# Performance work log

Measured on AMD Instinct MI355X. Metric: run time of the kernel, lower is better.

## Reference

```python
import jax, jax.numpy as jnp
import numpy as np

PHI = (1.0 + np.sqrt(5.0)) / 2.0
B, S, D, N, L, H, V = 2, 1024, 128, 256, 2, 2, 32000


def _euler_scan(w_emb, b_emb, positions):
    # w_emb, b_emb: (B,S,D); sequential complex-rotation recurrence over S
    Bq, Sq, Dq = w_emb.shape

    def step(carry, xs):
        h_real, h_imag = carry
        w_t, b_t, pos = xs  # (B,D), (B,D), ()
        wl = 1.0 + jnp.abs(w_t)
        t_phi = pos * PHI
        th_r = h_real / wl + b_t + t_phi
        th_i = h_imag / wl + b_t + t_phi
        sr, cr = jnp.sin(th_r), jnp.cos(th_r)
        si, ci = jnp.sin(th_i), jnp.cos(th_i)
        nr = cr * ci - sr * si
        ni = cr * si + sr * ci
        return (nr, ni), (nr, ni)

    init = (jnp.zeros((Bq, Dq), w_emb.dtype), jnp.zeros((Bq, Dq), w_emb.dtype))
    xs = (jnp.swapaxes(w_emb, 0, 1), jnp.swapaxes(b_emb, 0, 1), positions)
    _, (reals, imags) = jax.lax.scan(step, init, xs)
    return jnp.swapaxes(reals, 0, 1), jnp.swapaxes(imags, 0, 1)


def _echo_head(states_real, states_imag, positions, w_q, b_q, alpha_p):
    Bq, Sq, Dq = states_real.shape
    scale = jnp.sqrt(jnp.asarray(2.0 * Dq, states_real.dtype))
    wl_q = 1.0 + jnp.abs(w_q)
    t_phi = (positions * PHI)[None, :, None]
    th_r = states_real / wl_q + b_q + t_phi
    th_i = states_imag / wl_q + b_q + t_phi
    Q = jnp.concatenate([jnp.cos(th_r), jnp.cos(th_i)], axis=-1)  # (B,S,2D)
    K = jnp.concatenate([states_real, states_imag], axis=-1)      # (B,S,2D)
    scores = jnp.einsum('bqd,bkd->bqk', Q, K) / scale
    causal = jnp.triu(jnp.ones((Sq, Sq), bool), k=1)
    scores = jnp.where(causal[None], -jnp.inf, scores)
    scores = scores.at[:, 0, 0].set(0.0)
    attn = jax.nn.softmax(scores, axis=-1)
    retrieved = jnp.einsum('bqk,bkd->bqd', attn, K)  # (B,S,2D)
    alpha = jax.nn.sigmoid(alpha_p)

    def ema_step(ema, x_t):
        ema = alpha * x_t + (1.0 - alpha) * ema
        return ema, ema

    _, ema_states = jax.lax.scan(ema_step,
                                 jnp.zeros((Bq, 2 * Dq), retrieved.dtype),
                                 jnp.swapaxes(retrieved, 0, 1))
    ema_states = jnp.swapaxes(ema_states, 0, 1)  # (B,S,2D)
    return ema_states[..., :Dq] + ema_states[..., Dq:]


def _echo_module(states_real, states_imag, positions, w_q, b_q, alpha_p, w_out, b_out):
    # w_q,b_q: (H,D); alpha_p: (H,)
    heads = jax.vmap(_echo_head, in_axes=(None, None, None, 0, 0, 0))(
        states_real, states_imag, positions, w_q, b_q, alpha_p)
    combined = heads.sum(axis=0)  # interference sum over heads
    wl_out = 1.0 + jnp.abs(w_out)
    theta = combined / wl_out + b_out
    return jnp.cos(theta) + jnp.sin(theta)


def _resonant_ffn(x, W, Bp, attn_cos, attn_sin, proj_cos, proj_sin):
    # x: (B,S,D); W,Bp,attn_*: (N,D); proj_*: (D,N)
    theta = x[..., None, :] / (1.0 + jnp.abs(W)) + Bp  # (B,S,N,D)
    cos_sum = jnp.sum(jnp.cos(theta) * attn_cos, axis=-1)  # (B,S,N)
    sin_sum = jnp.sum(jnp.sin(theta) * attn_sin, axis=-1)
    out = cos_sum @ proj_cos.T + sin_sum @ proj_sin.T  # (B,S,D)
    return jax.nn.silu(out)


def setup_inputs() -> dict:
    key = jax.random.key(0)
    ks = jax.random.split(key, 16)
    f32 = jnp.float32
    return {
        'input_ids': jax.random.randint(ks[0], (B, S), 0, V),
        'embed': jax.random.normal(ks[1], (V, 2 * D), f32) * 0.02,
        'wq': jax.random.normal(ks[2], (L, H, D), f32) * 0.02,
        'bq': jnp.zeros((L, H, D), f32),
        'alpha': jnp.full((L, H), 0.1, f32),
        'wout': jax.random.normal(ks[3], (L, D), f32) * 0.02,
        'bout': jnp.zeros((L, D), f32),
        'ffn_W': jax.random.normal(ks[4], (L, N, D), f32) * 0.02,
        'ffn_B': jnp.zeros((L, N, D), f32),
        'attn_cos': jnp.ones((L, N, D), f32),
        'attn_sin': jnp.ones((L, N, D), f32),
        'proj_cos': jax.random.uniform(ks[5], (L, D, N), f32, -0.05, 0.05),
        'proj_sin': jax.random.uniform(ks[6], (L, D, N), f32, -0.05, 0.05),
        'echo_scales': jnp.full((L,), 0.5, f32),
        'res_scales': jnp.full((L,), 0.5, f32),
        'out_proj': jax.random.normal(ks[7], (V, D), f32) * 0.02,
    }


def reference(input_ids, embed, wq, bq, alpha, wout, bout, ffn_W, ffn_B,
              attn_cos, attn_sin, proj_cos, proj_sin, echo_scales, res_scales,
              out_proj):
    emb = embed[input_ids]  # (B,S,2D)
    Dq = emb.shape[-1] // 2
    w_emb, b_emb = emb[..., :Dq], emb[..., Dq:]
    positions = jnp.arange(emb.shape[1], dtype=emb.dtype)
    sr, si = _euler_scan(w_emb, b_emb, positions)
    x = sr + si
    for l in range(wq.shape[0]):
        echo = _echo_module(sr, si, positions, wq[l], bq[l], alpha[l], wout[l], bout[l])
        res = _resonant_ffn(x, ffn_W[l], ffn_B[l], attn_cos[l], attn_sin[l],
                            proj_cos[l], proj_sin[l])
        x = x + (echo_scales[l] * echo + res_scales[l] * res)
    return x @ out_proj.T  # (B,S,V)
```

## Files before the change

kernel.cpp:

```cpp
#include <hip/hip_runtime.h>
#include <math.h>

#define B_ 2
#define S_ 1024
#define D_ 128
#define N_ 256
#define L_ 2
#define H_ 2
#define V_ 32000

#define INV2PI 0.15915494309189535f
#define PHI_F 1.61803398874989484f

__device__ __forceinline__ float fract_(float x) { return x - floorf(x); }
__device__ __forceinline__ float fsin_(float th) { return __builtin_amdgcn_sinf(fract_(th * INV2PI)); }
__device__ __forceinline__ float fcos_(float th) { return __builtin_amdgcn_cosf(fract_(th * INV2PI)); }

typedef __bf16 bf16x8 __attribute__((ext_vector_type(8)));
typedef float f32x4 __attribute__((ext_vector_type(4)));

__global__ __launch_bounds__(256) void k_gp(const int* __restrict__ ids, const float* __restrict__ embed,
                                            float* __restrict__ eg,
                                            const float* __restrict__ W, const float* __restrict__ Bp,
                                            const float* __restrict__ ac, const float* __restrict__ as2,
                                            const float* __restrict__ pc, const float* __restrict__ ps,
                                            float* __restrict__ iwT, float* __restrict__ bpT,
                                            float* __restrict__ acT, float* __restrict__ asT,
                                            float* __restrict__ pcT, float* __restrict__ psT) {
    int blk = blockIdx.x;
    if (blk < 2048) {
        int i = blk * 256 + threadIdx.x;
        int c = i & 255, t = (i >> 8) & 1023, b = i >> 18;
        eg[i] = embed[(size_t)ids[b * S_ + t] * 256 + c];
    } else {
        int i = (blk - 2048) * 256 + threadIdx.x;
        int d = i & 127, n = (i >> 7) & 255, l = i >> 15;
        int ti = (l * 128 + d) * 256 + n;
        iwT[ti] = 1.f / (1.f + fabsf(W[i]));
        bpT[ti] = Bp[i];
        acT[ti] = ac[i];
        asT[ti] = as2[i];
        pcT[(l * 256 + n) * 128 + d] = pc[ti];
        psT[(l * 256 + n) * 128 + d] = ps[ti];
    }
}

__global__ __launch_bounds__(128) void k_euler(const float* __restrict__ eg,
                                               float* __restrict__ sr, float* __restrict__ si,
                                               float* __restrict__ x,
                                               __bf16* __restrict__ Kh, __bf16* __restrict__ Kl,
                                               __bf16* __restrict__ KTh, __bf16* __restrict__ KTl) {
    int b = blockIdx.x;
    int d = threadIdx.x;
    const float* p0 = eg + (size_t)b * S_ * 256 + d;
    float h = 0.f;
    double tp = 0.0;
    const double DTP = 2.0 * 1.6180339887498949;
    const double TWO_PI = 6.283185307179586476925286766559;
    float wA[8], bA[8], wB[8], bB[8];
#pragma unroll
    for (int k = 0; k < 8; ++k) { wA[k] = p0[k * 256]; bA[k] = p0[k * 256 + 128]; }
    for (int g = 0; g < 128; ++g) {
        if (g < 127) {
            const float* p = p0 + (size_t)(g + 1) * 8 * 256;
#pragma unroll
            for (int k = 0; k < 8; ++k) { wB[k] = p[k * 256]; bB[k] = p[k * 256 + 128]; }
        }
#pragma unroll
        for (int k = 0; k < 8; ++k) {
            int t = g * 8 + k;
            float inv = 1.f / (1.f + fabsf(wA[k]));
            float th = fmaf(h, inv, 2.f * bA[k] + (float)tp);
            float u = fract_(th * INV2PI);
            float sn = __builtin_amdgcn_sinf(u);
            float cs = __builtin_amdgcn_cosf(u);
            size_t idx = ((size_t)b * S_ + t) * D_ + d;
            sr[idx] = cs; si[idx] = sn; x[idx] = cs + sn;
            __bf16 ch = (__bf16)cs; __bf16 cl = (__bf16)(cs - (float)ch);
            __bf16 sh2 = (__bf16)sn; __bf16 sl = (__bf16)(sn - (float)sh2);
            size_t ki = ((size_t)b * S_ + t) * 256 + d;
            Kh[ki] = ch; Kl[ki] = cl;
            Kh[ki + 128] = sh2; Kl[ki + 128] = sl;
            size_t kt1 = ((size_t)b * 256 + d) * S_ + t;
            size_t kt2 = ((size_t)b * 256 + d + 128) * S_ + t;
            KTh[kt1] = ch; KTl[kt1] = cl;
            KTh[kt2] = sh2; KTl[kt2] = sl;
            h = cs + sn;
            tp += DTP; if (tp >= TWO_PI) tp -= TWO_PI;
        }
#pragma unroll
        for (int k = 0; k < 8; ++k) { wA[k] = wB[k]; bA[k] = bB[k]; }
    }
}

__global__ __launch_bounds__(256) void k_qq(const float* __restrict__ sr, const float* __restrict__ si,
                                            const float* __restrict__ wq, const float* __restrict__ bq,
                                            __bf16* __restrict__ Qh0, __bf16* __restrict__ Ql0,
                                            __bf16* __restrict__ Qh1, __bf16* __restrict__ Ql1) {
    int i = blockIdx.x * 256 + threadIdx.x;
    int l = i >> 20;
    int j = i & 0xFFFFF;
    int c = j & 255;
    int s = (j >> 8) & 1023;
    int bh = j >> 18;
    int h = bh & 1, b = bh >> 1;
    int d = c & 127;
    const float* st = (c < 128) ? sr : si;
    float v = st[((size_t)b * S_ + s) * D_ + d];
    float w = wq[(l * H_ + h) * D_ + d], bb = bq[(l * H_ + h) * D_ + d];
    float th = v / (1.f + fabsf(w)) + bb + (float)s * PHI_F;
    float qv = fcos_(th);
    __bf16 hq = (__bf16)qv;
    __bf16 lq = (__bf16)(qv - (float)hq);
    if (l == 0) { Qh0[j] = hq; Ql0[j] = lq; }
    else        { Qh1[j] = hq; Ql1[j] = lq; }
}

#define LSTR 40

__global__ __launch_bounds__(256) void k_scores_mfma(const __bf16* __restrict__ Qh, const __bf16* __restrict__ Ql,
                                                     const __bf16* __restrict__ Kh, const __bf16* __restrict__ Kl,
                                                     float* __restrict__ sc) {
    int kt = blockIdx.x, qt = blockIdx.y, bh = blockIdx.z;
    if (kt > qt) return;
    __shared__ __bf16 Ah[128 * LSTR], Al[128 * LSTR], Bh[128 * LSTR], Bl[128 * LSTR];
    int tid = threadIdx.x;
    int wid = tid >> 6, lane = tid & 63;
    int wy = wid >> 1, wx = wid & 1;
    int fl = lane & 15, qq = lane >> 4;
    int srow = tid >> 1, sseg = (tid & 1) * 16;
    const __bf16* qh = Qh + ((size_t)bh * S_ + qt * 128 + srow) * 256 + sseg;
    const __bf16* ql = Ql + ((size_t)bh * S_ + qt * 128 + srow) * 256 + sseg;
    const __bf16* kh = Kh + ((size_t)(bh >> 1) * S_ + kt * 128 + srow) * 256 + sseg;
    const __bf16* kl = Kl + ((size_t)(bh >> 1) * S_ + kt * 128 + srow) * 256 + sseg;
    int lbase = srow * LSTR + sseg;

    f32x4 acc[4][4];
#pragma unroll
    for (int i = 0; i < 4; ++i)
#pragma unroll
        for (int j = 0; j < 4; ++j) { acc[i][j][0] = 0.f; acc[i][j][1] = 0.f; acc[i][j][2] = 0.f; acc[i][j][3] = 0.f; }

    for (int kc = 0; kc < 256; kc += 32) {
        uint4 a0 = *(const uint4*)(qh + kc); uint4 a1 = *(const uint4*)(qh + kc + 8);
        uint4 l0 = *(const uint4*)(ql + kc); uint4 l1 = *(const uint4*)(ql + kc + 8);
        uint4 b0 = *(const uint4*)(kh + kc); uint4 b1 = *(const uint4*)(kh + kc + 8);
        uint4 c0 = *(const uint4*)(kl + kc); uint4 c1 = *(const uint4*)(kl + kc + 8);
        __syncthreads();
        *(uint4*)&Ah[lbase] = a0; *(uint4*)&Ah[lbase + 8] = a1;
        *(uint4*)&Al[lbase] = l0; *(uint4*)&Al[lbase + 8] = l1;
        *(uint4*)&Bh[lbase] = b0; *(uint4*)&Bh[lbase + 8] = b1;
        *(uint4*)&Bl[lbase] = c0; *(uint4*)&Bl[lbase + 8] = c1;
        __syncthreads();
        bf16x8 fah[4], fal[4], fbh[4], fbl[4];
#pragma unroll
        for (int tm = 0; tm < 4; ++tm) {
            int r = (wy * 64 + tm * 16 + fl) * LSTR + qq * 8;
            fah[tm] = *(const bf16x8*)&Ah[r];
            fal[tm] = *(const bf16x8*)&Al[r];
        }
#pragma unroll
        for (int tn = 0; tn < 4; ++tn) {
            int r = (wx * 64 + tn * 16 + fl) * LSTR + qq * 8;
            fbh[tn] = *(const bf16x8*)&Bh[r];
            fbl[tn] = *(const bf16x8*)&Bl[r];
        }
#pragma unroll
        for (int tm = 0; tm < 4; ++tm)
#pragma unroll
            for (int tn = 0; tn < 4; ++tn) {
                acc[tm][tn] = __builtin_amdgcn_mfma_f32_16x16x32_bf16(fah[tm], fbh[tn], acc[tm][tn], 0, 0, 0);
                acc[tm][tn] = __builtin_amdgcn_mfma_f32_16x16x32_bf16(fah[tm], fbl[tn], acc[tm][tn], 0, 0, 0);
                acc[tm][tn] = __builtin_amdgcn_mfma_f32_16x16x32_bf16(fal[tm], fbh[tn], acc[tm][tn], 0, 0, 0);
            }
    }
    const float s16 = 0.0625f;
    float* Cp = sc + (size_t)bh * S_ * S_;
    int grow0 = qt * 128 + wy * 64 + qq * 4;
    int gcol0 = kt * 128 + wx * 64 + fl;
#pragma unroll
    for (int tm = 0; tm < 4; ++tm)
#pragma unroll
        for (int tn = 0; tn < 4; ++tn) {
            size_t base = (size_t)(grow0 + tm * 16) * S_ + gcol0 + tn * 16;
#pragma unroll
            for (int r = 0; r < 4; ++r)
                Cp[base + (size_t)r * S_] = acc[tm][tn][r] * s16;
        }
}

__global__ __launch_bounds__(256) void k_pv_sm(const float* __restrict__ SCf,
                                               const __bf16* __restrict__ KTh, const __bf16* __restrict__ KTl,
                                               float* __restrict__ R) {
    __shared__ __bf16 Ah[128 * LSTR], Al[128 * LSTR], Bh[128 * LSTR], Bl[128 * LSTR];
    __shared__ float mrow[128], rrow[128];
    int nt = blockIdx.x, qt = blockIdx.y, bh = blockIdx.z;
    int tid = threadIdx.x;
    int wid = tid >> 6, lane = tid & 63;
    int wy = wid >> 1, wx = wid & 1;
    int fl = lane & 15, qq = lane >> 4;
    int srow = tid >> 1, half = tid & 1, sseg = half * 16;
    const float* Sp = SCf + (size_t)bh * S_ * S_;
    int kceil = qt * 128 + 128;
    {
        int r = srow;
        int q = qt * 128 + r;
        const float* rp = Sp + (size_t)q * S_;
        float m = -3e38f;
        for (int c = half * 4; c < kceil; c += 8) {
            float4 v = *(const float4*)&rp[c];
            if (c + 0 <= q) m = fmaxf(m, v.x);
            if (c + 1 <= q) m = fmaxf(m, v.y);
            if (c + 2 <= q) m = fmaxf(m, v.z);
            if (c + 3 <= q) m = fmaxf(m, v.w);
        }
        m = fmaxf(m, __shfl_xor(m, 1));
        float s = 0.f;
        for (int c = half * 4; c < kceil; c += 8) {
            float4 v = *(const float4*)&rp[c];
            if (c + 0 <= q) s += __expf(v.x - m);
            if (c + 1 <= q) s += __expf(v.y - m);
            if (c + 2 <= q) s += __expf(v.z - m);
            if (c + 3 <= q) s += __expf(v.w - m);
        }
        s += __shfl_xor(s, 1);
        mrow[r] = m;
        rrow[r] = 1.f / s;
    }
    __syncthreads();
    float mR = mrow[srow], rsR = rrow[srow];
    int qrow = qt * 128 + srow;
    const float* ap = Sp + (size_t)qrow * S_ + sseg;
    const __bf16* bh_p = KTh + ((size_t)(bh >> 1) * 256 + nt * 128 + srow) * S_ + sseg;
    const __bf16* bl_p = KTl + ((size_t)(bh >> 1) * 256 + nt * 128 + srow) * S_ + sseg;
    int lbase = srow * LSTR + sseg;

    f32x4 acc[4][4];
#pragma unroll
    for (int i = 0; i < 4; ++i)
#pragma unroll
        for (int j = 0; j < 4; ++j) { acc[i][j][0] = 0.f; acc[i][j][1] = 0.f; acc[i][j][2] = 0.f; acc[i][j][3] = 0.f; }

    for (int kc = 0; kc < kceil; kc += 32) {
        float4 f0 = *(const float4*)(ap + kc);
        float4 f1 = *(const float4*)(ap + kc + 4);
        float4 f2 = *(const float4*)(ap + kc + 8);
        float4 f3 = *(const float4*)(ap + kc + 12);
        uint4 b0 = *(const uint4*)(bh_p + kc); uint4 b1 = *(const uint4*)(bh_p + kc + 8);
        uint4 c0 = *(const uint4*)(bl_p + kc); uint4 c1 = *(const uint4*)(bl_p + kc + 8);
        float vv[16] = {f0.x, f0.y, f0.z, f0.w, f1.x, f1.y, f1.z, f1.w,
                        f2.x, f2.y, f2.z, f2.w, f3.x, f3.y, f3.z, f3.w};
        bf16x8 h0, h1, l0, l1;
#pragma unroll
        for (int e = 0; e < 16; ++e) {
            int col = kc + sseg + e;
            float p = (col <= qrow) ? __expf(vv[e] - mR) * rsR : 0.f;
            __bf16 hi = (__bf16)p;
            __bf16 lo = (__bf16)(p - (float)hi);
            if (e < 8) { h0[e] = hi; l0[e] = lo; }
            else       { h1[e - 8] = hi; l1[e - 8] = lo; }
        }
        __syncthreads();
        *(bf16x8*)&Ah[lbase] = h0; *(bf16x8*)&Ah[lbase + 8] = h1;
        *(bf16x8*)&Al[lbase] = l0; *(bf16x8*)&Al[lbase + 8] = l1;
        *(uint4*)&Bh[lbase] = b0; *(uint4*)&Bh[lbase + 8] = b1;
        *(uint4*)&Bl[lbase] = c0; *(uint4*)&Bl[lbase + 8] = c1;
        __syncthreads();
        bf16x8 fah[4], fal[4], fbh[4], fbl[4];
#pragma unroll
        for (int tm = 0; tm < 4; ++tm) {
            int r = (wy * 64 + tm * 16 + fl) * LSTR + qq * 8;
            fah[tm] = *(const bf16x8*)&Ah[r];
            fal[tm] = *(const bf16x8*)&Al[r];
        }
#pragma unroll
        for (int tn = 0; tn < 4; ++tn) {
            int r = (wx * 64 + tn * 16 + fl) * LSTR + qq * 8;
            fbh[tn] = *(const bf16x8*)&Bh[r];
            fbl[tn] = *(const bf16x8*)&Bl[r];
        }
#pragma unroll
        for (int tm = 0; tm < 4; ++tm)
#pragma unroll
            for (int tn = 0; tn < 4; ++tn) {
                acc[tm][tn] = __builtin_amdgcn_mfma_f32_16x16x32_bf16(fah[tm], fbh[tn], acc[tm][tn], 0, 0, 0);
                acc[tm][tn] = __builtin_amdgcn_mfma_f32_16x16x32_bf16(fah[tm], fbl[tn], acc[tm][tn], 0, 0, 0);
                acc[tm][tn] = __builtin_amdgcn_mfma_f32_16x16x32_bf16(fal[tm], fbh[tn], acc[tm][tn], 0, 0, 0);
            }
    }
    float* Rp = R + (size_t)bh * S_ * 256;
    int grow0 = qt * 128 + wy * 64 + qq * 4;
    int gcol0 = nt * 128 + wx * 64 + fl;
#pragma unroll
    for (int tm = 0; tm < 4; ++tm)
#pragma unroll
        for (int tn = 0; tn < 4; ++tn) {
            size_t base = (size_t)(grow0 + tm * 16) * 256 + gcol0 + tn * 16;
#pragma unroll
            for (int r = 0; r < 4; ++r)
                Rp[base + (size_t)r * 256] = acc[tm][tn][r];
        }
}

#define TROWS 4
__global__ __launch_bounds__(256) void k_tail(const float* __restrict__ R,
                                              const float* __restrict__ apar,
                                              float* __restrict__ x,
                                              const float* __restrict__ iwT, const float* __restrict__ bpT,
                                              const float* __restrict__ acT, const float* __restrict__ asT,
                                              const float* __restrict__ pcT, const float* __restrict__ psT,
                                              const float* __restrict__ wout, const float* __restrict__ bout,
                                              const float* __restrict__ esp, const float* __restrict__ rsp,
                                              __bf16* __restrict__ Xh, __bf16* __restrict__ Xl, int last) {
    int blk = blockIdx.x;
    int row0 = blk * TROWS;
    int b = row0 >> 10, t0 = row0 & 1023;
    int tid = threadIdx.x;
    __shared__ float wsh[2][64];
    __shared__ float emah[TROWS][256];
    __shared__ float xs[TROWS][128];
    __shared__ float csh[TROWS][256], ssh[TROWS][256];
    if (tid < 128) {
        int h = tid >> 6, j = tid & 63;
        float a = 1.f / (1.f + __expf(-apar[h]));
        wsh[h][j] = a * exp2f((float)j * log2f(1.f - a));
    }
    {
        int i0 = tid;
        xs[i0 >> 7][i0 & 127] = x[(size_t)row0 * D_ + i0];
        int i1 = tid + 256;
        xs[i1 >> 7][i1 & 127] = x[(size_t)row0 * D_ + i1];
    }
    __syncthreads();
    {
        int dim = tid;
        if (t0 >= 63) {
#pragma unroll
            for (int r = 0; r < TROWS; ++r) {
                int t = t0 + r;
                float acc = 0.f;
#pragma unroll
                for (int h = 0; h < 2; ++h) {
                    const float* base = R + ((size_t)(b * 2 + h) * S_ + t) * 256 + dim;
                    float s = 0.f;
#pragma unroll
                    for (int j = 0; j < 64; ++j) s = fmaf(wsh[h][j], base[-j * 256], s);
                    acc += s;
                }
                emah[r][dim] = acc;
            }
        } else {
            for (int r = 0; r < TROWS; ++r) {
                int t = t0 + r;
                int jm = t < 63 ? t : 63;
                float acc = 0.f;
                for (int h = 0; h < 2; ++h) {
                    const float* base = R + ((size_t)(b * 2 + h) * S_ + t) * 256 + dim;
                    float s = 0.f;
                    for (int j = 0; j <= jm; ++j) s = fmaf(wsh[h][j], base[-j * 256], s);
                    acc += s;
                }
                emah[r][dim] = acc;
            }
        }
    }
    __syncthreads();
    {
        int n = tid;
        float ac_[TROWS] = {}, as_[TROWS] = {};
        for (int d = 0; d < 128; ++d) {
            float iw = iwT[d * 256 + n];
            float bp = bpT[d * 256 + n];
            float wc = acT[d * 256 + n];
            float ws2 = asT[d * 256 + n];
#pragma unroll
            for (int r = 0; r < TROWS; ++r) {
                float th = fmaf(xs[r][d], iw, bp);
                float u = fract_(th * INV2PI);
                ac_[r] = fmaf(__builtin_amdgcn_cosf(u), wc, ac_[r]);
                as_[r] = fmaf(__builtin_amdgcn_sinf(u), ws2, as_[r]);
            }
        }
#pragma unroll
        for (int r = 0; r < TROWS; ++r) { csh[r][n] = ac_[r]; ssh[r][n] = as_[r]; }
    }
    __syncthreads();
    {
        int g = tid >> 7, d = tid & 127;
        float a0 = 0.f, a1 = 0.f;
        for (int nn = 0; nn < 256; ++nn) {
            float pc = pcT[nn * 128 + d], ps = psT[nn * 128 + d];
            a0 = fmaf(csh[g * 2 + 0][nn], pc, fmaf(ssh[g * 2 + 0][nn], ps, a0));
            a1 = fmaf(csh[g * 2 + 1][nn], pc, fmaf(ssh[g * 2 + 1][nn], ps, a1));
        }
        float es = esp[0], rs = rsp[0];
        float wl = 1.f + fabsf(wout[d]);
        float bo = bout[d];
#pragma unroll
        for (int rr = 0; rr < 2; ++rr) {
            int r = g * 2 + rr;
            float v = rr ? a1 : a0;
            float res = v / (1.f + __expf(-v));
            float comb = emah[r][d] + emah[r][d + 128];
            float th = comb / wl + bo;
            float u = fract_(th * INV2PI);
            float echo = __builtin_amdgcn_cosf(u) + __builtin_amdgcn_sinf(u);
            size_t gi = (size_t)(row0 + r) * D_ + d;
            float xn = xs[r][d] + es * echo + rs * res;
            x[gi] = xn;
            if (last) {
                __bf16 hi = (__bf16)xn;
                Xh[gi] = hi;
                Xl[gi] = (__bf16)(xn - (float)hi);
            }
        }
    }
}

__global__ __launch_bounds__(256) void k_out_mfma(const __bf16* __restrict__ Xh, const __bf16* __restrict__ Xl,
                                                  const float* __restrict__ P,
                                                  float* __restrict__ out) {
    __shared__ __bf16 Ah[128 * LSTR], Al[128 * LSTR], Bh[128 * LSTR], Bl[128 * LSTR];
    int mt = blockIdx.x, nt = blockIdx.y;
    int tid = threadIdx.x;
    int wid = tid >> 6, lane = tid & 63;
    int wy = wid >> 1, wx = wid & 1;
    int fl = lane & 15, q = lane >> 4;
    int srow = tid >> 1, sseg = (tid & 1) * 16;
    const __bf16* xh = Xh + (size_t)(mt * 128 + srow) * 128 + sseg;
    const __bf16* xl = Xl + (size_t)(mt * 128 + srow) * 128 + sseg;
    const float* pf = P + (size_t)(nt * 128 + srow) * 128 + sseg;
    int lbase = srow * LSTR + sseg;

    f32x4 acc[4][4];
#pragma unroll
    for (int i = 0; i < 4; ++i)
#pragma unroll
        for (int j = 0; j < 4; ++j) { acc[i][j][0] = 0.f; acc[i][j][1] = 0.f; acc[i][j][2] = 0.f; acc[i][j][3] = 0.f; }

    for (int kc = 0; kc < 128; kc += 32) {
        uint4 vxh0 = *(const uint4*)(xh + kc); uint4 vxh1 = *(const uint4*)(xh + kc + 8);
        uint4 vxl0 = *(const uint4*)(xl + kc); uint4 vxl1 = *(const uint4*)(xl + kc + 8);
        float4 p0 = *(const float4*)(pf + kc);
        float4 p1 = *(const float4*)(pf + kc + 4);
        float4 p2 = *(const float4*)(pf + kc + 8);
        float4 p3 = *(const float4*)(pf + kc + 12);
        float pv_[16] = {p0.x, p0.y, p0.z, p0.w, p1.x, p1.y, p1.z, p1.w,
                         p2.x, p2.y, p2.z, p2.w, p3.x, p3.y, p3.z, p3.w};
        bf16x8 bh0, bh1, bl0, bl1;
#pragma unroll
        for (int e = 0; e < 16; ++e) {
            __bf16 hi = (__bf16)pv_[e];
            __bf16 lo = (__bf16)(pv_[e] - (float)hi);
            if (e < 8) { bh0[e] = hi; bl0[e] = lo; }
            else       { bh1[e - 8] = hi; bl1[e - 8] = lo; }
        }
        __syncthreads();
        *(uint4*)&Ah[lbase] = vxh0; *(uint4*)&Ah[lbase + 8] = vxh1;
        *(uint4*)&Al[lbase] = vxl0; *(uint4*)&Al[lbase + 8] = vxl1;
        *(bf16x8*)&Bh[lbase] = bh0; *(bf16x8*)&Bh[lbase + 8] = bh1;
        *(bf16x8*)&Bl[lbase] = bl0; *(bf16x8*)&Bl[lbase + 8] = bl1;
        __syncthreads();
        bf16x8 ah[4], al[4], bh[4], bl[4];
#pragma unroll
        for (int tm = 0; tm < 4; ++tm) {
            int r = (wy * 64 + tm * 16 + fl) * LSTR + q * 8;
            ah[tm] = *(const bf16x8*)&Ah[r];
            al[tm] = *(const bf16x8*)&Al[r];
        }
#pragma unroll
        for (int tn = 0; tn < 4; ++tn) {
            int r = (wx * 64 + tn * 16 + fl) * LSTR + q * 8;
            bh[tn] = *(const bf16x8*)&Bh[r];
            bl[tn] = *(const bf16x8*)&Bl[r];
        }
#pragma unroll
        for (int tm = 0; tm < 4; ++tm)
#pragma unroll
            for (int tn = 0; tn < 4; ++tn) {
                acc[tm][tn] = __builtin_amdgcn_mfma_f32_16x16x32_bf16(ah[tm], bh[tn], acc[tm][tn], 0, 0, 0);
                acc[tm][tn] = __builtin_amdgcn_mfma_f32_16x16x32_bf16(ah[tm], bl[tn], acc[tm][tn], 0, 0, 0);
                acc[tm][tn] = __builtin_amdgcn_mfma_f32_16x16x32_bf16(al[tm], bh[tn], acc[tm][tn], 0, 0, 0);
            }
    }
    int grow0 = mt * 128 + wy * 64 + q * 4;
    int gcol0 = nt * 128 + wx * 64 + fl;
#pragma unroll
    for (int tm = 0; tm < 4; ++tm)
#pragma unroll
        for (int tn = 0; tn < 4; ++tn) {
            size_t base = (size_t)(grow0 + tm * 16) * V_ + gcol0 + tn * 16;
#pragma unroll
            for (int r = 0; r < 4; ++r)
                out[base + (size_t)r * V_] = acc[tm][tn][r];
        }
}

extern "C" void kernel_launch(void* const* d_in, const int* in_sizes, int n_in,
                              void* d_out, int out_size, void* d_ws, size_t ws_size,
                              hipStream_t stream) {
    const int* ids = (const int*)d_in[0];
    const float* embed = (const float*)d_in[1];
    const float* wq = (const float*)d_in[2];
    const float* bq = (const float*)d_in[3];
    const float* alpha = (const float*)d_in[4];
    const float* wout = (const float*)d_in[5];
    const float* bout = (const float*)d_in[6];
    const float* ffnW = (const float*)d_in[7];
    const float* ffnB = (const float*)d_in[8];
    const float* acos_ = (const float*)d_in[9];
    const float* asin_ = (const float*)d_in[10];
    const float* pcos = (const float*)d_in[11];
    const float* psin = (const float*)d_in[12];
    const float* escl = (const float*)d_in[13];
    const float* rscl = (const float*)d_in[14];
    const float* oprj = (const float*)d_in[15];
    float* out = (float*)d_out;
    float* ws = (float*)d_ws;

    float* EG = ws;
    float* SR = EG + 524288;
    float* SI = SR + 262144;
    float* X  = SI + 262144;
    float* KB = X + 262144;
    float* Q0 = KB + 524288;
    float* SC = Q0 + 1048576;
    float* RT = SC + 4194304;
    float* KT = RT + 1048576;
    float* Q1 = KT + 524288;
    float* T_IW = Q1 + 1048576;
    float* T_BP = T_IW + 65536;
    float* T_AC = T_BP + 65536;
    float* T_AS = T_AC + 65536;
    float* T_PC = T_AS + 65536;
    float* T_PS = T_PC + 65536;
    __bf16* KH = (__bf16*)KB;
    __bf16* KL = KH + 524288;
    __bf16* QH0 = (__bf16*)Q0;
    __bf16* QL0 = QH0 + 1048576;
    __bf16* QH1 = (__bf16*)Q1;
    __bf16* QL1 = QH1 + 1048576;
    __bf16* KTH = (__bf16*)KT;
    __bf16* KTL = KTH + 524288;
    __bf16* XH = (__bf16*)SC;
    __bf16* XL = XH + 262144;

    k_gp<<<2304, 256, 0, stream>>>(ids, embed, EG, ffnW, ffnB, acos_, asin_, pcos, psin,
                                   T_IW, T_BP, T_AC, T_AS, T_PC, T_PS);
    k_euler<<<2, 128, 0, stream>>>(EG, SR, SI, X, KH, KL, KTH, KTL);
    k_qq<<<8192, 256, 0, stream>>>(SR, SI, wq, bq, QH0, QL0, QH1, QL1);

    for (int l = 0; l < L_; ++l) {
        k_scores_mfma<<<dim3(8, 8, 4), 256, 0, stream>>>(l ? QH1 : QH0, l ? QL1 : QL0, KH, KL, SC);
        k_pv_sm<<<dim3(2, 8, 4), 256, 0, stream>>>(SC, KTH, KTL, RT);
        k_tail<<<512, 256, 0, stream>>>(RT, alpha + l * H_, X,
                                        T_IW + l * 32768, T_BP + l * 32768,
                                        T_AC + l * 32768, T_AS + l * 32768,
                                        T_PC + l * 32768, T_PS + l * 32768,
                                        wout + l * D_, bout + l * D_,
                                        escl + l, rscl + l, XH, XL, l == L_ - 1);
    }
    k_out_mfma<<<dim3(16, 250), 256, 0, stream>>>(XH, XL, oprj, out);
}
```

Baseline: 901.4 us.

## Move K/KT bf16 split and transpose out of serial euler scan into parallel kernel

The sequential euler recurrence kernel, running only 2 blocks, now writes just the cos/sin states. A new tiled kernel reads them back and produces x, the hi/lo bf16 K buffers, and the transposed KT buffers through a shared-memory transpose for coalesced stores. This takes the strided transposed stores off the latency-bound serial path, at the cost of an extra launch and a re-read of sr/si.

```diff
diff --git a/kernel.cpp b/kernel.cpp
--- a/kernel.cpp
+++ b/kernel.cpp
@@ -46,13 +46,12 @@
 }
 
 __global__ __launch_bounds__(128) void k_euler(const float* __restrict__ eg,
-                                               float* __restrict__ sr, float* __restrict__ si,
-                                               float* __restrict__ x,
-                                               __bf16* __restrict__ Kh, __bf16* __restrict__ Kl,
-                                               __bf16* __restrict__ KTh, __bf16* __restrict__ KTl) {
+                                               float* __restrict__ sr, float* __restrict__ si) {
     int b = blockIdx.x;
     int d = threadIdx.x;
     const float* p0 = eg + (size_t)b * S_ * 256 + d;
+    float* srp = sr + (size_t)b * S_ * D_ + d;
+    float* sip = si + (size_t)b * S_ * D_ + d;
     float h = 0.f;
     double tp = 0.0;
     const double DTP = 2.0 * 1.6180339887498949;
@@ -74,22 +73,51 @@
             float u = fract_(th * INV2PI);
             float sn = __builtin_amdgcn_sinf(u);
             float cs = __builtin_amdgcn_cosf(u);
-            size_t idx = ((size_t)b * S_ + t) * D_ + d;
-            sr[idx] = cs; si[idx] = sn; x[idx] = cs + sn;
-            __bf16 ch = (__bf16)cs; __bf16 cl = (__bf16)(cs - (float)ch);
-            __bf16 sh2 = (__bf16)sn; __bf16 sl = (__bf16)(sn - (float)sh2);
-            size_t ki = ((size_t)b * S_ + t) * 256 + d;
-            Kh[ki] = ch; Kl[ki] = cl;
-            Kh[ki + 128] = sh2; Kl[ki + 128] = sl;
-            size_t kt1 = ((size_t)b * 256 + d) * S_ + t;
-            size_t kt2 = ((size_t)b * 256 + d + 128) * S_ + t;
-            KTh[kt1] = ch; KTl[kt1] = cl;
-            KTh[kt2] = sh2; KTl[kt2] = sl;
+            srp[(size_t)t * D_] = cs;
+            sip[(size_t)t * D_] = sn;
             h = cs + sn;
             tp += DTP; if (tp >= TWO_PI) tp -= TWO_PI;
         }
 #pragma unroll
         for (int k = 0; k < 8; ++k) { wA[k] = wB[k]; bA[k] = bB[k]; }
+    }
+}
+
+__global__ __launch_bounds__(256) void k_fan(const float* __restrict__ sr, const float* __restrict__ si,
+                                             float* __restrict__ x,
+                                             __bf16* __restrict__ Kh, __bf16* __restrict__ Kl,
+                                             __bf16* __restrict__ KTh, __bf16* __restrict__ KTl) {
+    __shared__ float tc[32][33], ts[32][33];
+    int b = blockIdx.z;
+    int t0 = blockIdx.x * 32, d0 = blockIdx.y * 32;
+    int lx = threadIdx.x & 31, ly = threadIdx.x >> 5;
+#pragma unroll
+    for (int i = 0; i < 4; ++i) {
+        int tr = ly + i * 8;
+        int t = t0 + tr;
+        size_t si_ = ((size_t)b * S_ + t) * D_ + d0 + lx;
+        float cs = sr[si_];
+        float sn = si[si_];
+        tc[tr][lx] = cs; ts[tr][lx] = sn;
+        x[si_] = cs + sn;
+        __bf16 ch = (__bf16)cs; __bf16 cl = (__bf16)(cs - (float)ch);
+        __bf16 sh2 = (__bf16)sn; __bf16 sl = (__bf16)(sn - (float)sh2);
+        size_t ki = ((size_t)b * S_ + t) * 256 + d0 + lx;
+        Kh[ki] = ch; Kl[ki] = cl;
+        Kh[ki + 128] = sh2; Kl[ki + 128] = sl;
+    }
+    __syncthreads();
+#pragma unroll
+    for (int i = 0; i < 4; ++i) {
+        int dr = ly + i * 8;
+        int d = d0 + dr;
+        float cs = tc[lx][dr], sn = ts[lx][dr];
+        __bf16 ch = (__bf16)cs; __bf16 cl = (__bf16)(cs - (float)ch);
+        __bf16 sh2 = (__bf16)sn; __bf16 sl = (__bf16)(sn - (float)sh2);
+        size_t k1 = ((size_t)b * 256 + d) * S_ + t0 + lx;
+        size_t k2 = ((size_t)b * 256 + d + 128) * S_ + t0 + lx;
+        KTh[k1] = ch; KTl[k1] = cl;
+        KTh[k2] = sh2; KTl[k2] = sl;
     }
 }
 
@@ -547,7 +575,8 @@
 
     k_gp<<<2304, 256, 0, stream>>>(ids, embed, EG, ffnW, ffnB, acos_, asin_, pcos, psin,
                                    T_IW, T_BP, T_AC, T_AS, T_PC, T_PS);
-    k_euler<<<2, 128, 0, stream>>>(EG, SR, SI, X, KH, KL, KTH, KTL);
+    k_euler<<<2, 128, 0, stream>>>(EG, SR, SI);
+    k_fan<<<dim3(32, 4, 2), 256, 0, stream>>>(SR, SI, X, KH, KL, KTH, KTL);
     k_qq<<<8192, 256, 0, stream>>>(SR, SI, wq, bq, QH0, QL0, QH1, QL1);
 
     for (int l = 0; l < L_; ++l) {
```

Result: faster. 831.3 us (-7.8%).
